# Kernel optimization log

Hardware: AMD Instinct MI355X
Metric: run time of the kernel (lower is better)

The kernel has to match this reference:

```python
import jax, jax.numpy as jnp
import numpy as np

N_NODE = 50000
N_MOL = 1024
C_DIM = 128
M_DIM = 128
P_DIM = 64
RADIUS = 2
NEG_INF = -1e9


def _leaky(x):
    return jnp.where(x > 0, x, 0.01 * x)


def setup_inputs() -> dict:
    key = jax.random.key(0)
    ks = jax.random.split(key, 16)
    node_features = jax.random.normal(ks[0], (N_NODE, C_DIM), dtype=jnp.float32)
    pos_features = jax.random.normal(ks[1], (N_NODE, P_DIM), dtype=jnp.float32)
    # each node assigned to one molecule -> dense bipartite assignment matrix
    assign = np.arange(N_NODE) % N_MOL
    mat = np.zeros((N_MOL, N_NODE), dtype=np.float32)
    mat[assign, np.arange(N_NODE)] = 1.0
    mask = np.where(mat > 0, 0.0, NEG_INF).astype(np.float32)
    s = 0.05
    params = dict(
        map_W=jax.random.normal(ks[2], (M_DIM, C_DIM), dtype=jnp.float32) * s,
        map_b=jnp.zeros((M_DIM,), dtype=jnp.float32),
        attend_W=jax.random.normal(ks[3], (C_DIM, C_DIM + P_DIM), dtype=jnp.float32) * s,
        attend_b=jnp.zeros((C_DIM,), dtype=jnp.float32),
        align_W=jax.random.normal(ks[4], (1, M_DIM + C_DIM + P_DIM), dtype=jnp.float32) * s,
        align_b=jnp.zeros((1,), dtype=jnp.float32),
        gru_Wih=jax.random.normal(ks[5], (3 * M_DIM, C_DIM), dtype=jnp.float32) * s,
        gru_Whh=jax.random.normal(ks[6], (3 * M_DIM, M_DIM), dtype=jnp.float32) * s,
        gru_bih=jnp.zeros((3 * M_DIM,), dtype=jnp.float32),
        gru_bhh=jnp.zeros((3 * M_DIM,), dtype=jnp.float32),
    )
    return dict(node_features=node_features, pos_features=pos_features,
                mol_node_matrix=jnp.asarray(mat), mol_node_mask=jnp.asarray(mask),
                **params)


def _gru_cell(x, h, Wih, Whh, bih, bhh):
    gi = x @ Wih.T + bih          # [M, 3*m_dim]
    gh = h @ Whh.T + bhh
    ir, iz, inn = jnp.split(gi, 3, axis=-1)
    hr, hz, hn = jnp.split(gh, 3, axis=-1)
    r = jax.nn.sigmoid(ir + hr)
    z = jax.nn.sigmoid(iz + hz)
    n = jnp.tanh(inn + r * hn)
    return (1.0 - z) * n + z * h


def reference(node_features, pos_features, mol_node_matrix, mol_node_mask,
              map_W, map_b, attend_W, attend_b, align_W, align_b,
              gru_Wih, gru_Whh, gru_bih, gru_bhh):
    # mol_features: [M, m_dim]
    mol_features = mol_node_matrix @ _leaky(node_features @ map_W.T + map_b)
    np_cat = jnp.concatenate([node_features, pos_features], axis=-1)  # [N, c+p]
    for _ in range(RADIUS):
        h = np_cat @ attend_W.T + attend_b                            # [N, c_dim] (dropout p=0)
        node_mol = mol_node_matrix.T @ mol_features                   # [N, m_dim]
        a = _leaky(jnp.concatenate([node_mol, pos_features, node_features], -1)
                   @ align_W.T + align_b)                             # [N, 1]
        # mol_node_matrix @ diag(a) == column scaling (avoids O(N^2) diag)
        logits = mol_node_matrix * a[:, 0][None, :] + mol_node_mask   # [M, N]
        w = jax.nn.softmax(logits, axis=1)
        context = jax.nn.elu(w @ h)                                   # [M, c_dim]
        mol_features = jax.nn.relu(
            _gru_cell(context, mol_features, gru_Wih, gru_Whh, gru_bih, gru_bhh))
    return mol_features
```

## Files before the change

### kernel.cpp

```cpp
#include <hip/hip_runtime.h>
#include <hip/hip_bf16.h>
#include <math.h>

#define N_NODE 50000
#define N_MOL  1024
#define C_DIM  128
#define P_DIM  64
#define M_DIM  128
#define NM_REM 848
#define NVBLK  196

typedef __attribute__((ext_vector_type(8))) short bf16x8;
typedef __attribute__((ext_vector_type(4))) float f32x4;

static __device__ __forceinline__ short f2bf(float x) {
    __hip_bfloat16 h = __float2bfloat16(x);
    return *reinterpret_cast<short*>(&h);
}
static __device__ __forceinline__ float bfs2f(short s) {
    unsigned int u = ((unsigned int)(unsigned short)s) << 16;
    float f;
    __builtin_memcpy(&f, &u, 4);
    return f;
}
static __device__ __forceinline__ int off_of(int m) {
    return (m < NM_REM) ? 49 * m : NM_REM + 48 * m;
}

__global__ __launch_bounds__(256) void k_prep_guess(const float* __restrict__ mat,
                                                    const float* __restrict__ map_W,
                                                    const float* __restrict__ att_W,
                                                    const float* __restrict__ Wih,
                                                    const float* __restrict__ Whh,
                                                    const float* __restrict__ alignW,
                                                    short* __restrict__ Bbf,
                                                    short* __restrict__ Wihb,
                                                    short* __restrict__ Whhb,
                                                    int* __restrict__ list,
                                                    int* __restrict__ offsets,
                                                    int* __restrict__ flags) {
    const int NB = 272 * 192;
    const int NW = 384 * 128;
    int idx = blockIdx.x * 256 + threadIdx.x;
    if (idx < NB) {
        int r = idx / 192, k = idx - r * 192;
        float v = 0.f;
        if (r < 128) { if (k < 128) v = map_W[r * 128 + k]; }
        else if (r < 256) v = att_W[(size_t)(r - 128) * 192 + k];
        else if (r == 256) v = (k < 128) ? alignW[192 + k] : alignW[k];
        Bbf[idx] = f2bf(v);
    } else if (idx < NB + NW) {
        int j = idx - NB;
        Wihb[j] = f2bf(Wih[j]);
    } else if (idx < NB + 2 * NW) {
        int j = idx - NB - NW;
        Whhb[j] = f2bf(Whh[j]);
    }
    if (idx <= N_MOL) offsets[idx] = off_of(idx);
    if (idx < N_NODE) {
        int m = idx & (N_MOL - 1);
        list[off_of(m) + (idx >> 10)] = idx;
    }
    if (blockIdx.x < NVBLK) {
        __shared__ int s_bad;
        if (threadIdx.x == 0) s_bad = 0;
        __syncthreads();
        if (idx < N_NODE) {
            int m = idx & (N_MOL - 1);
            if (!(mat[(size_t)m * N_NODE + idx] > 0.5f)) atomicOr(&s_bad, 1);
        }
        __syncthreads();
        if (threadIdx.x == 0) flags[blockIdx.x] = s_bad;
    }
}

__global__ __launch_bounds__(1024) void k_fallback(const float4* __restrict__ mat4,
                                                   const int* __restrict__ flags,
                                                   int* __restrict__ assign,
                                                   int* __restrict__ offsets,
                                                   int* __restrict__ list) {
    __shared__ int s_any;
    __shared__ int s_scan[N_MOL];
    __shared__ int s_tile[4096];
    int t = threadIdx.x;
    if (t == 0) s_any = 0;
    __syncthreads();
    if (t < NVBLK && flags[t]) atomicOr(&s_any, 1);
    __syncthreads();
    if (s_any == 0) return;

    const int total4 = (N_MOL * N_NODE) / 4;
    for (int j = t; j < total4; j += 1024) {
        float4 v = mat4[j];
        float f[4] = {v.x, v.y, v.z, v.w};
#pragma unroll
        for (int c = 0; c < 4; ++c) {
            if (f[c] > 0.5f) {
                int idx = j * 4 + c;
                int m = idx / N_NODE;
                assign[idx - m * N_NODE] = m;
            }
        }
    }
    __syncthreads();
    s_scan[t] = 0;
    __syncthreads();
    for (int i = t; i < N_NODE; i += 1024) atomicAdd(&s_scan[assign[i]], 1);
    __syncthreads();
    for (int d = 1; d < N_MOL; d <<= 1) {
        int v = (t >= d) ? s_scan[t - d] : 0;
        __syncthreads();
        s_scan[t] += v;
        __syncthreads();
    }
    offsets[t + 1] = s_scan[t];
    if (t == 0) offsets[0] = 0;
    int base_off = (t == 0) ? 0 : s_scan[t - 1];
    __syncthreads();
    int cur = 0;
    for (int tb = 0; tb < N_NODE; tb += 4096) {
        for (int q = t; q < 4096; q += 1024)
            s_tile[q] = (tb + q < N_NODE) ? assign[tb + q] : -1;
        __syncthreads();
        int lim = (N_NODE - tb < 4096) ? (N_NODE - tb) : 4096;
        for (int q = 0; q < lim; ++q)
            if (s_tile[q] == t) list[base_off + (cur++)] = tb + q;
        __syncthreads();
    }
}

__global__ __launch_bounds__(256) void k_gemm_fused(const float* __restrict__ node,
                                                    const float* __restrict__ pos,
                                                    const int* __restrict__ list,
                                                    const short* __restrict__ Bbf,
                                                    const float* __restrict__ map_b,
                                                    const float* __restrict__ att_b,
                                                    __hip_bfloat16* __restrict__ mapped,
                                                    __hip_bfloat16* __restrict__ hbuf,
                                                    float* __restrict__ sbase) {
    __shared__ short sA[64 * 224];
    __shared__ int s_list[64];
    int t = threadIdx.x;
    int n0 = blockIdx.x * 64;

    if (t < 64) {
        int pr = n0 + t;
        s_list[t] = (pr < N_NODE) ? list[pr] : 0;
    }
    __syncthreads();

    for (int idx = t; idx < 64 * 48; idx += 256) {
        int row = idx / 48;
        int c4 = idx - row * 48;
        float4 v = make_float4(0.f, 0.f, 0.f, 0.f);
        if (n0 + row < N_NODE) {
            int id = s_list[row];
            if (c4 < 32) v = *(const float4*)&node[(size_t)id * C_DIM + c4 * 4];
            else         v = *(const float4*)&pos[(size_t)id * P_DIM + (c4 - 32) * 4];
        }
        ushort4 u;
        u.x = (unsigned short)f2bf(v.x);
        u.y = (unsigned short)f2bf(v.y);
        u.z = (unsigned short)f2bf(v.z);
        u.w = (unsigned short)f2bf(v.w);
        *(ushort4*)&sA[row * 224 + c4 * 4] = u;
    }
    __syncthreads();

    int wid = t >> 6, lane = t & 63;
    int wr = wid >> 1, wc = wid & 1;
    int lrow = lane & 15, lk = (lane >> 4) * 8;

    bf16x8 a[2][6];
#pragma unroll
    for (int mt = 0; mt < 2; ++mt)
#pragma unroll
        for (int k = 0; k < 6; ++k)
            a[mt][k] = *(const bf16x8*)&sA[(wr * 32 + mt * 16 + lrow) * 224 + k * 32 + lk];

    f32x4 acc[2][9] = {};
#pragma unroll
    for (int ct = 0; ct < 9; ++ct) {
        if (ct == 8 && wc == 0) break;
        int c0 = wc * 128 + ct * 16;
        bf16x8 b[6];
#pragma unroll
        for (int k = 0; k < 6; ++k)
            b[k] = *(const bf16x8*)&Bbf[(size_t)(c0 + lrow) * 192 + k * 32 + lk];
#pragma unroll
        for (int mt = 0; mt < 2; ++mt)
#pragma unroll
            for (int k = 0; k < 6; ++k)
                acc[mt][ct] = __builtin_amdgcn_mfma_f32_16x16x32_bf16(
                    a[mt][k], b[k], acc[mt][ct], 0, 0, 0);
    }

#pragma unroll
    for (int ct = 0; ct < 8; ++ct) {
        int c = wc * 128 + ct * 16 + lrow;
        float bias = (c < 128) ? map_b[c] : att_b[c - 128];
#pragma unroll
        for (int mt = 0; mt < 2; ++mt) {
#pragma unroll
            for (int r = 0; r < 4; ++r) {
                int pr = n0 + wr * 32 + mt * 16 + (lane >> 4) * 4 + r;
                if (pr >= N_NODE) continue;
                float v = acc[mt][ct][r] + bias;
                if (c < 128) {
                    v = (v > 0.f) ? v : 0.01f * v;
                    mapped[(size_t)pr * 128 + c] = __float2bfloat16(v);
                } else {
                    hbuf[(size_t)pr * 128 + (c - 128)] = __float2bfloat16(v);
                }
            }
        }
    }
    if (wc == 1 && lrow == 0) {
#pragma unroll
        for (int mt = 0; mt < 2; ++mt)
#pragma unroll
            for (int r = 0; r < 4; ++r) {
                int pr = n0 + wr * 32 + mt * 16 + (lane >> 4) * 4 + r;
                if (pr < N_NODE) sbase[pr] = acc[mt][8][r];
            }
    }
}

__global__ __launch_bounds__(256) void k_molrad(const __hip_bfloat16* __restrict__ mapped,
                                                const __hip_bfloat16* __restrict__ hbuf,
                                                const float* __restrict__ sbase,
                                                const float* __restrict__ alignW,
                                                const float* __restrict__ alignb,
                                                const short* __restrict__ Wihb,
                                                const short* __restrict__ Whhb,
                                                const float* __restrict__ bih,
                                                const float* __restrict__ bhh,
                                                const int* __restrict__ offsets,
                                                float* __restrict__ mol) {
    __shared__ short s_actx[16][136];
    __shared__ short s_amol[16][136];
    __shared__ float s_molf[4][128];
    __shared__ float s_gi[4][384];
    __shared__ float s_gh[4][384];
    int t = threadIdx.x;
    int w = t >> 6, lane = t & 63;
    int m0 = blockIdx.x * 4;
    int mymol = m0 + w;

    for (int i = t; i < 12 * 128; i += 256) {
        int r = 4 + (i >> 7), c = i & 127;
        s_actx[r][c] = 0;
        s_amol[r][c] = 0;
    }

    int off = offsets[mymol];
    int cnt = offsets[mymol + 1] - off;
    int Q = cnt * 16;

    const short* mbase = (const short*)mapped + (size_t)off * 128;
    float acc8[8] = {};
    for (int q = lane; q < Q; q += 64) {
        bf16x8 v = *(const bf16x8*)&mbase[q * 8];
#pragma unroll
        for (int jj = 0; jj < 8; ++jj) acc8[jj] += bfs2f(v[jj]);
    }
#pragma unroll
    for (int jj = 0; jj < 8; ++jj) {
        acc8[jj] += __shfl_xor(acc8[jj], 16);
        acc8[jj] += __shfl_xor(acc8[jj], 32);
    }
    if (lane < 16) {
#pragma unroll
        for (int jj = 0; jj < 8; ++jj) {
            int c = lane * 8 + jj;
            s_molf[w][c] = acc8[jj];
            s_amol[w][c] = f2bf(acc8[jj]);
        }
    }
    float aw0 = alignW[lane], aw1 = alignW[64 + lane];
    float ab = alignb[0];
    int lrow = lane & 15, lk = (lane >> 4) * 8;
    __syncthreads();

    for (int it = 0; it < 2; ++it) {
        float v = s_molf[w][lane] * aw0 + s_molf[w][64 + lane] * aw1;
#pragma unroll
        for (int d = 32; d > 0; d >>= 1) v += __shfl_xor(v, d);
        float dm = v + ab;

        float x = -1e30f;
        if (lane < cnt) {
            x = sbase[off + lane] + dm;
            x = (x > 0.f) ? x : 0.01f * x;
        }
        float mx = x;
#pragma unroll
        for (int d = 32; d > 0; d >>= 1) mx = fmaxf(mx, __shfl_xor(mx, d));
        float e = (lane < cnt) ? __expf(x - mx) : 0.f;
        float sm = e;
#pragma unroll
        for (int d = 32; d > 0; d >>= 1) sm += __shfl_xor(sm, d);
        float myw = e / sm;

        const short* hb = (const short*)hbuf + (size_t)off * 128;
        float c8[8] = {};
        for (int q = lane; q < Q; q += 64) {
            bf16x8 vv = *(const bf16x8*)&hb[q * 8];
            float wgt = __shfl(myw, q >> 4);
#pragma unroll
            for (int jj = 0; jj < 8; ++jj) c8[jj] += wgt * bfs2f(vv[jj]);
        }
#pragma unroll
        for (int jj = 0; jj < 8; ++jj) {
            c8[jj] += __shfl_xor(c8[jj], 16);
            c8[jj] += __shfl_xor(c8[jj], 32);
        }
        if (lane < 16) {
#pragma unroll
            for (int jj = 0; jj < 8; ++jj) {
                float cv = c8[jj];
                cv = (cv > 0.f) ? cv : (__expf(cv) - 1.f);
                s_actx[w][lane * 8 + jj] = f2bf(cv);
            }
        }
        __syncthreads();

        bf16x8 a_c[4], a_m[4];
#pragma unroll
        for (int k = 0; k < 4; ++k) {
            a_c[k] = *(const bf16x8*)&s_actx[lrow][k * 32 + lk];
            a_m[k] = *(const bf16x8*)&s_amol[lrow][k * 32 + lk];
        }
#pragma unroll
        for (int j = 0; j < 6; ++j) {
            int c0 = w * 96 + j * 16;
            f32x4 ai = {}, ah = {};
#pragma unroll
            for (int k = 0; k < 4; ++k) {
                bf16x8 bi = *(const bf16x8*)&Wihb[(size_t)(c0 + lrow) * 128 + k * 32 + lk];
                ai = __builtin_amdgcn_mfma_f32_16x16x32_bf16(a_c[k], bi, ai, 0, 0, 0);
                bf16x8 bh = *(const bf16x8*)&Whhb[(size_t)(c0 + lrow) * 128 + k * 32 + lk];
                ah = __builtin_amdgcn_mfma_f32_16x16x32_bf16(a_m[k], bh, ah, 0, 0, 0);
            }
            if (lane < 16) {
#pragma unroll
                for (int r = 0; r < 4; ++r) {
                    s_gi[r][c0 + lane] = ai[r];
                    s_gh[r][c0 + lane] = ah[r];
                }
            }
        }
        __syncthreads();

#pragma unroll
        for (int j = 0; j < 2; ++j) {
            int item = t + j * 256;
            int mm = item >> 7, c = item & 127;
            float gir = s_gi[mm][c] + bih[c];
            float giz = s_gi[mm][128 + c] + bih[128 + c];
            float gin = s_gi[mm][256 + c] + bih[256 + c];
            float ghr = s_gh[mm][c] + bhh[c];
            float ghz = s_gh[mm][128 + c] + bhh[128 + c];
            float ghn = s_gh[mm][256 + c] + bhh[256 + c];
            float molc = s_molf[mm][c];
            float rr = 1.f / (1.f + __expf(-(gir + ghr)));
            float zz = 1.f / (1.f + __expf(-(giz + ghz)));
            float nn = tanhf(gin + rr * ghn);
            float o = fmaxf((1.f - zz) * nn + zz * molc, 0.f);
            s_molf[mm][c] = o;
            s_amol[mm][c] = f2bf(o);
        }
        __syncthreads();
    }

#pragma unroll
    for (int j = 0; j < 2; ++j) {
        int item = t + j * 256;
        int mm = item >> 7, c = item & 127;
        mol[(size_t)(m0 + mm) * 128 + c] = s_molf[mm][c];
    }
}

extern "C" void kernel_launch(void* const* d_in, const int* in_sizes, int n_in,
                              void* d_out, int out_size, void* d_ws, size_t ws_size,
                              hipStream_t stream) {
    const float* node   = (const float*)d_in[0];
    const float* pos    = (const float*)d_in[1];
    const float* mat    = (const float*)d_in[2];
    const float* map_W  = (const float*)d_in[4];
    const float* map_b  = (const float*)d_in[5];
    const float* att_W  = (const float*)d_in[6];
    const float* att_b  = (const float*)d_in[7];
    const float* alignW = (const float*)d_in[8];
    const float* alignb = (const float*)d_in[9];
    const float* gWih   = (const float*)d_in[10];
    const float* gWhh   = (const float*)d_in[11];
    const float* gbih   = (const float*)d_in[12];
    const float* gbhh   = (const float*)d_in[13];
    float* mol = (float*)d_out;

    size_t o = 0;
    auto alloc = [&](size_t bytes) { size_t r = o; o += (bytes + 255) & ~(size_t)255; return r; };
    char* ws = (char*)d_ws;
    int*   flags   = (int*)(ws + alloc((size_t)NVBLK * 4));
    int*   assign  = (int*)(ws + alloc((size_t)N_NODE * 4));
    int*   offsets = (int*)(ws + alloc((size_t)(N_MOL + 1) * 4));
    int*   list    = (int*)(ws + alloc((size_t)N_NODE * 4));
    short* Bbf     = (short*)(ws + alloc((size_t)272 * 192 * 2));
    short* Wihb    = (short*)(ws + alloc((size_t)384 * 128 * 2));
    short* Whhb    = (short*)(ws + alloc((size_t)384 * 128 * 2));
    __hip_bfloat16* mapped = (__hip_bfloat16*)(ws + alloc((size_t)N_NODE * 128 * 2));
    __hip_bfloat16* hbuf   = (__hip_bfloat16*)(ws + alloc((size_t)N_NODE * 128 * 2));
    float* sbase   = (float*)(ws + alloc((size_t)N_NODE * 4));

    int prep_items = 272 * 192 + 2 * 384 * 128;
    k_prep_guess<<<(prep_items + 255) / 256, 256, 0, stream>>>(
        mat, map_W, att_W, gWih, gWhh, alignW, Bbf, Wihb, Whhb, list, offsets, flags);
    k_fallback<<<1, 1024, 0, stream>>>((const float4*)mat, flags,
                                       assign, offsets, list);
    k_gemm_fused<<<(N_NODE + 63) / 64, 256, 0, stream>>>(node, pos, list, Bbf,
                                                         map_b, att_b,
                                                         mapped, hbuf, sbase);
    k_molrad<<<N_MOL / 4, 256, 0, stream>>>(mapped, hbuf, sbase, alignW, alignb,
                                            Wihb, Whhb, gbih, gbhh, offsets, mol);
}
```

Measured before the change: 93.32 us.

## Stage GEMM epilogue through LDS for coalesced stores; fuse GRU gates in registers

In the fused node GEMM, results are now written as bf16 into a padded shared-memory tile and then copied out with 16-byte vectorized, row-contiguous stores. Before, each lane wrote scattered 2-byte values, so global writes were poorly coalesced. In the molecule GRU kernel, each wave's output columns are remapped so it owns matching r/z/n gate channels. The gate math then runs directly on MFMA accumulators, which removes the s_gi/s_gh shared buffers and one pass through shared memory. The trade-offs are extra barriers, a larger LDS tile, and only 16 active lanes in the GRU gate computation.

```diff
diff --git a/kernel.cpp b/kernel.cpp
--- a/kernel.cpp
+++ b/kernel.cpp
@@ -138,7 +138,7 @@
                                                     __hip_bfloat16* __restrict__ mapped,
                                                     __hip_bfloat16* __restrict__ hbuf,
                                                     float* __restrict__ sbase) {
-    __shared__ short sA[64 * 224];
+    __shared__ short smem[64 * 264];
     __shared__ int s_list[64];
     int t = threadIdx.x;
     int n0 = blockIdx.x * 64;
@@ -163,7 +163,7 @@
         u.y = (unsigned short)f2bf(v.y);
         u.z = (unsigned short)f2bf(v.z);
         u.w = (unsigned short)f2bf(v.w);
-        *(ushort4*)&sA[row * 224 + c4 * 4] = u;
+        *(ushort4*)&smem[row * 264 + c4 * 4] = u;
     }
     __syncthreads();
 
@@ -176,7 +176,7 @@
     for (int mt = 0; mt < 2; ++mt)
 #pragma unroll
         for (int k = 0; k < 6; ++k)
-            a[mt][k] = *(const bf16x8*)&sA[(wr * 32 + mt * 16 + lrow) * 224 + k * 32 + lk];
+            a[mt][k] = *(const bf16x8*)&smem[(wr * 32 + mt * 16 + lrow) * 264 + k * 32 + lk];
 
     f32x4 acc[2][9] = {};
 #pragma unroll
@@ -195,6 +195,8 @@
                     a[mt][k], b[k], acc[mt][ct], 0, 0, 0);
     }
 
+    __syncthreads();
+
 #pragma unroll
     for (int ct = 0; ct < 8; ++ct) {
         int c = wc * 128 + ct * 16 + lrow;
@@ -203,15 +205,10 @@
         for (int mt = 0; mt < 2; ++mt) {
 #pragma unroll
             for (int r = 0; r < 4; ++r) {
-                int pr = n0 + wr * 32 + mt * 16 + (lane >> 4) * 4 + r;
-                if (pr >= N_NODE) continue;
+                int row = wr * 32 + mt * 16 + (lane >> 4) * 4 + r;
                 float v = acc[mt][ct][r] + bias;
-                if (c < 128) {
-                    v = (v > 0.f) ? v : 0.01f * v;
-                    mapped[(size_t)pr * 128 + c] = __float2bfloat16(v);
-                } else {
-                    hbuf[(size_t)pr * 128 + (c - 128)] = __float2bfloat16(v);
-                }
+                if (c < 128) v = (v > 0.f) ? v : 0.01f * v;
+                smem[row * 264 + c] = f2bf(v);
             }
         }
     }
@@ -223,6 +220,24 @@
                 int pr = n0 + wr * 32 + mt * 16 + (lane >> 4) * 4 + r;
                 if (pr < N_NODE) sbase[pr] = acc[mt][8][r];
             }
+    }
+    __syncthreads();
+
+    short* mp = (short*)mapped;
+    short* hp = (short*)hbuf;
+    for (int v = t; v < 64 * 16; v += 256) {
+        int row = v >> 4, ch = v & 15;
+        int pr = n0 + row;
+        if (pr < N_NODE)
+            *(bf16x8*)&mp[(size_t)pr * 128 + ch * 8] =
+                *(const bf16x8*)&smem[row * 264 + ch * 8];
+    }
+    for (int v = t; v < 64 * 16; v += 256) {
+        int row = v >> 4, ch = v & 15;
+        int pr = n0 + row;
+        if (pr < N_NODE)
+            *(bf16x8*)&hp[(size_t)pr * 128 + ch * 8] =
+                *(const bf16x8*)&smem[row * 264 + 128 + ch * 8];
     }
 }
 
@@ -240,8 +255,6 @@
     __shared__ short s_actx[16][136];
     __shared__ short s_amol[16][136];
     __shared__ float s_molf[4][128];
-    __shared__ float s_gi[4][384];
-    __shared__ float s_gh[4][384];
     int t = threadIdx.x;
     int w = t >> 6, lane = t & 63;
     int m0 = blockIdx.x * 4;
@@ -331,44 +344,45 @@
             a_c[k] = *(const bf16x8*)&s_actx[lrow][k * 32 + lk];
             a_m[k] = *(const bf16x8*)&s_amol[lrow][k * 32 + lk];
         }
+        f32x4 ai[6], ah[6];
+#pragma unroll
+        for (int j = 0; j < 6; ++j) { ai[j] = (f32x4){}; ah[j] = (f32x4){}; }
 #pragma unroll
         for (int j = 0; j < 6; ++j) {
-            int c0 = w * 96 + j * 16;
-            f32x4 ai = {}, ah = {};
+            int c0 = w * 32 + (j & 1) * 16 + (j >> 1) * 128;
 #pragma unroll
             for (int k = 0; k < 4; ++k) {
                 bf16x8 bi = *(const bf16x8*)&Wihb[(size_t)(c0 + lrow) * 128 + k * 32 + lk];
-                ai = __builtin_amdgcn_mfma_f32_16x16x32_bf16(a_c[k], bi, ai, 0, 0, 0);
+                ai[j] = __builtin_amdgcn_mfma_f32_16x16x32_bf16(a_c[k], bi, ai[j], 0, 0, 0);
                 bf16x8 bh = *(const bf16x8*)&Whhb[(size_t)(c0 + lrow) * 128 + k * 32 + lk];
-                ah = __builtin_amdgcn_mfma_f32_16x16x32_bf16(a_m[k], bh, ah, 0, 0, 0);
-            }
-            if (lane < 16) {
+                ah[j] = __builtin_amdgcn_mfma_f32_16x16x32_bf16(a_m[k], bh, ah[j], 0, 0, 0);
+            }
+        }
+        __syncthreads();
+
+        if (lane < 16) {
+#pragma unroll
+            for (int j2 = 0; j2 < 2; ++j2) {
+                int chan = w * 32 + j2 * 16 + lane;
+                float br = bih[chan], bz = bih[128 + chan], bn = bih[256 + chan];
+                float cr = bhh[chan], cz = bhh[128 + chan], cn = bhh[256 + chan];
 #pragma unroll
                 for (int r = 0; r < 4; ++r) {
-                    s_gi[r][c0 + lane] = ai[r];
-                    s_gh[r][c0 + lane] = ah[r];
+                    float gir = ai[j2][r] + br;
+                    float giz = ai[2 + j2][r] + bz;
+                    float gin = ai[4 + j2][r] + bn;
+                    float ghr = ah[j2][r] + cr;
+                    float ghz = ah[2 + j2][r] + cz;
+                    float ghn = ah[4 + j2][r] + cn;
+                    float molc = s_molf[r][chan];
+                    float rr = 1.f / (1.f + __expf(-(gir + ghr)));
+                    float zz = 1.f / (1.f + __expf(-(giz + ghz)));
+                    float nn = tanhf(gin + rr * ghn);
+                    float o = fmaxf((1.f - zz) * nn + zz * molc, 0.f);
+                    s_molf[r][chan] = o;
+                    s_amol[r][chan] = f2bf(o);
                 }
             }
-        }
-        __syncthreads();
-
-#pragma unroll
-        for (int j = 0; j < 2; ++j) {
-            int item = t + j * 256;
-            int mm = item >> 7, c = item & 127;
-            float gir = s_gi[mm][c] + bih[c];
-            float giz = s_gi[mm][128 + c] + bih[128 + c];
-            float gin = s_gi[mm][256 + c] + bih[256 + c];
-            float ghr = s_gh[mm][c] + bhh[c];
-            float ghz = s_gh[mm][128 + c] + bhh[128 + c];
-            float ghn = s_gh[mm][256 + c] + bhh[256 + c];
-            float molc = s_molf[mm][c];
-            float rr = 1.f / (1.f + __expf(-(gir + ghr)));
-            float zz = 1.f / (1.f + __expf(-(giz + ghz)));
-            float nn = tanhf(gin + rr * ghn);
-            float o = fmaxf((1.f - zz) * nn + zz * molc, 0.f);
-            s_molf[mm][c] = o;
-            s_amol[mm][c] = f2bf(o);
         }
         __syncthreads();
     }
```

Measured after the change: 82.59 us. 1.13x faster.
